# Kernel optimization log

Hardware: AMD Instinct MI355X
Metric: run time of the kernel (lower is better)

Reference implementation:

```python
import jax, jax.numpy as jnp
import numpy as np

T, B = 128, 256      # seq_len, batch
D = 1024             # input_dim (embedding dim)
H = 1024             # hidden_dim
NQ = 8               # n_qubits
V = 32000            # vocab_size
TAGS = 1024          # tagset_size


def setup_inputs() -> dict:
    key = jax.random.key(0)
    ks = jax.random.split(key, 10)
    s = 0.05
    return {
        "sentence": jax.random.randint(ks[0], (T, B), 0, V),
        "emb": jax.random.normal(ks[1], (V, D), jnp.float32) * s,
        # gate order: forget, input, update, output (stacked on leading axis)
        "Wg": jax.random.normal(ks[2], (4, D + H, NQ), jnp.float32) * s,
        "bg": jax.random.normal(ks[3], (4, NQ), jnp.float32) * s,
        "theta": jax.random.normal(ks[4], (4, NQ), jnp.float32) * s,  # trainable RX angles
        "Wp": jax.random.normal(ks[5], (4, NQ, H), jnp.float32) * s,
        "bp": jax.random.normal(ks[6], (4, H), jnp.float32) * s,
        "W_tag": jax.random.normal(ks[7], (H, TAGS), jnp.float32) * s,
        "b_tag": jax.random.normal(ks[8], (TAGS,), jnp.float32) * s,
    }


def reference(sentence, emb, Wg, bg, theta, Wp, bp, W_tag, b_tag):
    embeds = emb[sentence]                      # (T, B, D)
    bsz = embeds.shape[1]
    hidden = Wp.shape[2]

    def step(carry, x):
        hx, cx = carry
        comb = jnp.concatenate([x, hx], axis=1)                       # (B, D+H)
        raw = jnp.einsum('bc,gcq->gbq', comb, Wg) + bg[:, None, :]    # (4, B, NQ)
        # QLayer: RX(x) then trainable RX(theta) per wire on |0>, measure Z
        # -> product state, <Z_i> = cos(raw_i + theta_i)  (exact)
        q = jnp.cos(raw + theta[:, None, :])                          # (4, B, NQ)
        proj = jnp.einsum('gbq,gqh->gbh', q, Wp) + bp[:, None, :]     # (4, B, H)
        f = jax.nn.sigmoid(proj[0])
        i = jax.nn.sigmoid(proj[1])
        g = jnp.tanh(proj[2])
        o = jax.nn.sigmoid(proj[3])
        cx = f * cx + i * g
        hx = o * jnp.tanh(cx)
        return (hx, cx), hx

    hx0 = jnp.zeros((bsz, hidden), embeds.dtype)
    cx0 = jnp.zeros((bsz, hidden), embeds.dtype)
    _, lstm_out = jax.lax.scan(step, (hx0, cx0), embeds)              # (T, B, H)
    tag_logits = lstm_out @ W_tag + b_tag                             # (T, B, TAGS)
    # torch applies log_softmax over dim=1 (the batch axis) -- faithful
    return jax.nn.log_softmax(tag_logits, axis=1)
```

## Files before the change

kernel.cpp:

```cpp
#include <hip/hip_runtime.h>
#include <hip/hip_bf16.h>
#include <stdint.h>

#define T_LEN 128
#define B_SZ  256
#define D_IN  1024
#define H_DIM 1024
#define NQ    8
#define VOCAB 32000
#define TAGS  1024

typedef __attribute__((ext_vector_type(8))) short short8;
typedef __attribute__((ext_vector_type(4))) float f32x4;

__device__ __forceinline__ unsigned short f2bf_bits(float x) {
    __hip_bfloat16 h = __float2bfloat16(x);
    unsigned short u; __builtin_memcpy(&u, &h, 2); return u;
}
__device__ __forceinline__ uint32_t pack_bf2(float a, float b) {
    return (uint32_t)f2bf_bits(a) | ((uint32_t)f2bf_bits(b) << 16);
}
__device__ __forceinline__ float sigmoid_f(float x) {
    return 1.f / (1.f + __expf(-x));
}
__device__ __forceinline__ float tanh_f(float x) {
    return 1.f - 2.f / (__expf(2.f * x) + 1.f);
}
__device__ __forceinline__ void gload_lds16(void* lds_base, const void* gptr) {
    __builtin_amdgcn_global_load_lds(
        (__attribute__((address_space(1))) const void*)gptr,
        (__attribute__((address_space(3))) void*)lds_base,
        16, 0, 0);
}

__global__ __launch_bounds__(256) void k_wt_transpose(const float* __restrict__ W,
                                                      __hip_bfloat16* __restrict__ WtT) {
    __shared__ float tile[32][33];
    const int kb = blockIdx.x * 32, nb = blockIdx.y * 32;
    const int r = threadIdx.x >> 5, c = threadIdx.x & 31;
#pragma unroll
    for (int i = 0; i < 4; ++i)
        tile[r + 8 * i][c] = W[(size_t)(kb + r + 8 * i) * TAGS + nb + c];
    __syncthreads();
#pragma unroll
    for (int i = 0; i < 4; ++i)
        WtT[(size_t)(nb + r + 8 * i) * H_DIM + kb + c] = __float2bfloat16(tile[c][r + 8 * i]);
}

#define GXB_ROWS 32
__global__ __launch_bounds__(256, 2) void k_gx(
    const int* __restrict__ sent, const float* __restrict__ emb,
    const float* __restrict__ Wg, const float* __restrict__ bg,
    const float* __restrict__ theta, float* __restrict__ gx)
{
    __shared__ float xs[2][1024];
    const int tid = threadIdx.x, lane = tid & 63, wv = tid >> 6;
    const int ol = lane & 7, s = lane >> 3;
    const int o = wv * 8 + ol;

    float wk[128];
#pragma unroll
    for (int k = 0; k < 32; ++k)
#pragma unroll
        for (int e = 0; e < 4; ++e) {
            const int c = (s + 8 * k) * 4 + e;
            wk[4 * k + e] = Wg[((size_t)wv * 2048 + c) * 8 + ol];
        }
    const float bt = bg[o] + theta[o];

    const int rbase = blockIdx.x * GXB_ROWS;
    const float4* emb4 = (const float4*)emb;
    float4 xn = emb4[(size_t)sent[rbase] * 256 + tid];
    *(float4*)&xs[0][4 * tid] = xn;
    __syncthreads();

    int cur = 0;
    for (int i8 = 0; i8 < GXB_ROWS / 8; ++i8) {
        float gacc[8];
#pragma unroll
        for (int ii = 0; ii < 8; ++ii) {
            const int i = i8 * 8 + ii;
            const bool havenext = (i + 1 < GXB_ROWS);
            if (havenext)
                xn = emb4[(size_t)sent[rbase + i + 1] * 256 + tid];

            const float4* x4 = (const float4*)xs[cur];
            float a0 = 0.f, a1 = 0.f, a2 = 0.f, a3 = 0.f;
#pragma unroll
            for (int k = 0; k < 32; ++k) {
                float4 v = x4[s + 8 * k];
                a0 = fmaf(wk[4 * k + 0], v.x, a0);
                a1 = fmaf(wk[4 * k + 1], v.y, a1);
                a2 = fmaf(wk[4 * k + 2], v.z, a2);
                a3 = fmaf(wk[4 * k + 3], v.w, a3);
            }
            float a = (a0 + a1) + (a2 + a3);
#pragma unroll
            for (int d = 8; d < 64; d <<= 1) a += __shfl_xor(a, d, 64);
            gacc[ii] = a + bt;

            if (havenext)
                *(float4*)&xs[cur ^ 1][4 * tid] = xn;
            __syncthreads();
            cur ^= 1;
        }
        if (lane < 8) {
#pragma unroll
            for (int ii = 0; ii < 8; ++ii)
                gx[(size_t)(rbase + i8 * 8 + ii) * 32 + wv * 8 + lane] = gacc[ii];
        }
    }
}

__global__ __launch_bounds__(256, 1) void k_qlstm(
    const float* __restrict__ gx, const float* __restrict__ Wg,
    const float* __restrict__ Wp, const float* __restrict__ bp,
    __hip_bfloat16* __restrict__ hb)
{
    __shared__ uint32_t hsb[512];
    __shared__ float red[4 * 36];
    __shared__ float gxl[T_LEN * 32];

    const int tid = threadIdx.x, lane = tid & 63, wv = tid >> 6;
    const int b = blockIdx.x;
    const int lg = lane >> 4;
    const int K0 = wv * 256;
    const int ol = lane & 31;

    union { short8 s8; uint32_t u[4]; } wf[2][8];
#pragma unroll
    for (int ro = 0; ro < 2; ++ro) {
        const int o = ro * 16 + (lane & 15);
        const int g = o >> 3, q = o & 7;
#pragma unroll
        for (int kt = 0; kt < 8; ++kt) {
            const int k0 = K0 + kt * 32 + lg * 8;
#pragma unroll
            for (int p = 0; p < 4; ++p) {
                float e0 = Wg[((size_t)g * 2048 + 1024 + k0 + 2 * p) * 8 + q];
                float e1 = Wg[((size_t)g * 2048 + 1024 + k0 + 2 * p + 1) * 8 + q];
                wf[ro][kt].u[p] = pack_bf2(e0, e1);
            }
        }
    }
    float wpv[4][32], bpv[4][4];
#pragma unroll
    for (int hh = 0; hh < 4; ++hh) {
#pragma unroll
        for (int j = 0; j < 32; ++j)
            wpv[hh][j] = Wp[(size_t)j * H_DIM + 4 * tid + hh];
#pragma unroll
        for (int gg = 0; gg < 4; ++gg)
            bpv[hh][gg] = bp[gg * H_DIM + 4 * tid + hh];
    }

    for (int i = tid; i < T_LEN * 32; i += 256)
        gxl[i] = gx[((size_t)(i >> 5) * B_SZ + b) * 32 + (i & 31)];

    *(uint2*)&hsb[2 * tid] = (uint2){0u, 0u};
    float cx0 = 0.f, cx1 = 0.f, cx2 = 0.f, cx3 = 0.f;
    __syncthreads();

    const f32x4 zf = (f32x4){0.f, 0.f, 0.f, 0.f};

    for (int t8 = 0; t8 < T_LEN / 8; ++t8) {
        uint2 hv8[8];
#pragma unroll
        for (int tt = 0; tt < 8; ++tt) {
            const int t = t8 * 8 + tt;

            f32x4 p0a = zf, p0b = zf, p1a = zf, p1b = zf;
#pragma unroll
            for (int kt = 0; kt < 8; kt += 2) {
                short8 bfA = *(const short8*)((const char*)hsb + 2 * K0 + 64 * kt + lg * 16);
                short8 bfB = *(const short8*)((const char*)hsb + 2 * K0 + 64 * (kt + 1) + lg * 16);
                p0a = __builtin_amdgcn_mfma_f32_16x16x32_bf16(wf[0][kt].s8, bfA, p0a, 0, 0, 0);
                p1a = __builtin_amdgcn_mfma_f32_16x16x32_bf16(wf[1][kt].s8, bfA, p1a, 0, 0, 0);
                p0b = __builtin_amdgcn_mfma_f32_16x16x32_bf16(wf[0][kt + 1].s8, bfB, p0b, 0, 0, 0);
                p1b = __builtin_amdgcn_mfma_f32_16x16x32_bf16(wf[1][kt + 1].s8, bfB, p1b, 0, 0, 0);
            }
            f32x4 p0 = p0a + p0b, p1 = p1a + p1b;
            if ((lane & 15) == 0) {
                *(f32x4*)&red[wv * 36 + 4 * lg] = p0;
                *(f32x4*)&red[wv * 36 + 16 + 4 * lg] = p1;
            }
            __syncthreads();

            float r = gxl[t * 32 + ol]
                    + red[0 * 36 + ol] + red[1 * 36 + ol]
                    + red[2 * 36 + ol] + red[3 * 36 + ol];
            const float qv = __cosf(r);
            float qa[32];
#pragma unroll
            for (int o = 0; o < 32; ++o) qa[o] = __shfl(qv, o, 64);

            float hv[4];
#pragma unroll
            for (int hh = 0; hh < 4; ++hh) {
                float pj[4];
#pragma unroll
                for (int gg = 0; gg < 4; ++gg) {
                    float s = bpv[hh][gg];
#pragma unroll
                    for (int j = 0; j < 8; ++j)
                        s = fmaf(qa[gg * 8 + j], wpv[hh][gg * 8 + j], s);
                    pj[gg] = s;
                }
                const float f_ = sigmoid_f(pj[0]);
                const float i_ = sigmoid_f(pj[1]);
                const float g_ = tanh_f(pj[2]);
                const float o_ = sigmoid_f(pj[3]);
                float& cx = (hh == 0) ? cx0 : (hh == 1) ? cx1 : (hh == 2) ? cx2 : cx3;
                cx = f_ * cx + i_ * g_;
                hv[hh] = o_ * tanh_f(cx);
            }
            const uint2 hvp = (uint2){pack_bf2(hv[0], hv[1]), pack_bf2(hv[2], hv[3])};
            *(uint2*)&hsb[2 * tid] = hvp;
            hv8[tt] = hvp;
            __syncthreads();
        }
#pragma unroll
        for (int tt = 0; tt < 8; ++tt)
            ((uint2*)hb)[((size_t)(t8 * 8 + tt) * B_SZ + b) * 256 + tid] = hv8[tt];
    }
}

__global__ __launch_bounds__(512) void k_tag_gemm_lsm(const __hip_bfloat16* __restrict__ Hb,
                                                      const __hip_bfloat16* __restrict__ WtT,
                                                      float* __restrict__ out)
{
    __shared__ short As[256 * 32];
    __shared__ short Bs[128 * 32];
    __shared__ float wred[8][64];
    __shared__ float wsum[8][64];

    const int t = blockIdx.x, n0 = blockIdx.y * 128;
    const int m0 = t * 256;
    const int tid = threadIdx.x, lane = tid & 63, wid = tid >> 6;
    const int wm = (wid & 3) * 64, wn = (wid >> 2) * 64;
    const int mrow = lane & 15, quad = lane >> 4;
    const int nh = wid >> 2, mw = wid & 3;

    const short* Hs = (const short*)Hb;
    const short* Ws = (const short*)WtT;

    f32x4 acc[4][4];
#pragma unroll
    for (int mi = 0; mi < 4; ++mi)
#pragma unroll
        for (int ni = 0; ni < 4; ++ni)
            acc[mi][ni] = (f32x4){0.f, 0.f, 0.f, 0.f};

    for (int kt = 0; kt < 32; ++kt) {
        const int k0 = kt * 32;
        __syncthreads();
#pragma unroll
        for (int rd = 0; rd < 2; ++rd) {
            const int c = wid + rd * 8;
            const int row = c * 16 + (lane >> 2);
            const int kc = (lane & 3) * 8;
            gload_lds16(&As[c * 512], &Hs[(size_t)(m0 + row) * H_DIM + k0 + kc]);
        }
        {
            const int c = wid;
            const int row = c * 16 + (lane >> 2);
            const int kc = (lane & 3) * 8;
            gload_lds16(&Bs[c * 512], &Ws[(size_t)(n0 + row) * H_DIM + k0 + kc]);
        }
        __syncthreads();

        short8 afr[4], bfr[4];
#pragma unroll
        for (int mi = 0; mi < 4; ++mi)
            afr[mi] = *(const short8*)&As[(wm + mi * 16 + mrow) * 32 + quad * 8];
#pragma unroll
        for (int ni = 0; ni < 4; ++ni)
            bfr[ni] = *(const short8*)&Bs[(wn + ni * 16 + mrow) * 32 + quad * 8];
#pragma unroll
        for (int mi = 0; mi < 4; ++mi)
#pragma unroll
            for (int ni = 0; ni < 4; ++ni)
                acc[mi][ni] = __builtin_amdgcn_mfma_f32_16x16x32_bf16(
                    afr[mi], bfr[ni], acc[mi][ni], 0, 0, 0);
    }

    float cmax[4];
#pragma unroll
    for (int ni = 0; ni < 4; ++ni) {
        float m = -1e30f;
#pragma unroll
        for (int mi = 0; mi < 4; ++mi)
#pragma unroll
            for (int r = 0; r < 4; ++r) m = fmaxf(m, acc[mi][ni][r]);
        m = fmaxf(m, __shfl_xor(m, 16, 64));
        m = fmaxf(m, __shfl_xor(m, 32, 64));
        cmax[ni] = m;
    }
    if (quad == 0) {
#pragma unroll
        for (int ni = 0; ni < 4; ++ni) wred[nh * 4 + mw][ni * 16 + mrow] = cmax[ni];
    }
    __syncthreads();
#pragma unroll
    for (int ni = 0; ni < 4; ++ni) {
        float m = wred[nh * 4 + 0][ni * 16 + mrow];
        m = fmaxf(m, wred[nh * 4 + 1][ni * 16 + mrow]);
        m = fmaxf(m, wred[nh * 4 + 2][ni * 16 + mrow]);
        m = fmaxf(m, wred[nh * 4 + 3][ni * 16 + mrow]);
        cmax[ni] = m;
    }
    float lse[4];
#pragma unroll
    for (int ni = 0; ni < 4; ++ni) {
        float s = 0.f;
#pragma unroll
        for (int mi = 0; mi < 4; ++mi)
#pragma unroll
            for (int r = 0; r < 4; ++r) s += __expf(acc[mi][ni][r] - cmax[ni]);
        s += __shfl_xor(s, 16, 64);
        s += __shfl_xor(s, 32, 64);
        lse[ni] = s;
    }
    if (quad == 0) {
#pragma unroll
        for (int ni = 0; ni < 4; ++ni) wsum[nh * 4 + mw][ni * 16 + mrow] = lse[ni];
    }
    __syncthreads();
#pragma unroll
    for (int ni = 0; ni < 4; ++ni) {
        const float s = wsum[nh * 4 + 0][ni * 16 + mrow]
                      + wsum[nh * 4 + 1][ni * 16 + mrow]
                      + wsum[nh * 4 + 2][ni * 16 + mrow]
                      + wsum[nh * 4 + 3][ni * 16 + mrow];
        lse[ni] = cmax[ni] + __logf(s);
    }
#pragma unroll
    for (int mi = 0; mi < 4; ++mi)
#pragma unroll
        for (int ni = 0; ni < 4; ++ni)
#pragma unroll
            for (int r = 0; r < 4; ++r) {
                const int grow = m0 + wm + mi * 16 + quad * 4 + r;
                const int gcol = n0 + wn + ni * 16 + mrow;
                out[(size_t)grow * TAGS + gcol] = acc[mi][ni][r] - lse[ni];
            }
}

extern "C" void kernel_launch(void* const* d_in, const int* in_sizes, int n_in,
                              void* d_out, int out_size, void* d_ws, size_t ws_size,
                              hipStream_t stream) {
    (void)in_sizes; (void)n_in; (void)out_size; (void)ws_size;
    const int*   sent  = (const int*)d_in[0];
    const float* emb   = (const float*)d_in[1];
    const float* Wg    = (const float*)d_in[2];
    const float* bg    = (const float*)d_in[3];
    const float* theta = (const float*)d_in[4];
    const float* Wp    = (const float*)d_in[5];
    const float* bp    = (const float*)d_in[6];
    const float* Wt    = (const float*)d_in[7];
    float* out = (float*)d_out;

    __hip_bfloat16* hb  = (__hip_bfloat16*)d_ws;
    __hip_bfloat16* WtT = (__hip_bfloat16*)((char*)d_ws + (size_t)64 * 1024 * 1024);
    float* gx = (float*)d_out;

    k_wt_transpose<<<dim3(32, 32), 256, 0, stream>>>(Wt, WtT);
    k_gx<<<dim3((T_LEN * B_SZ) / GXB_ROWS), 256, 0, stream>>>(sent, emb, Wg, bg, theta, gx);
    k_qlstm<<<dim3(B_SZ), 256, 0, stream>>>(gx, Wg, Wp, bp, hb);
    k_tag_gemm_lsm<<<dim3(T_LEN, TAGS / 128), 512, 0, stream>>>(hb, WtT, out);
}
```

Baseline: 574.3 us.

## Double qlstm block to 512 threads, halving per-thread hidden units and K slice

```diff
diff --git a/kernel.cpp b/kernel.cpp
--- a/kernel.cpp
+++ b/kernel.cpp
@@ -112,28 +112,28 @@
     }
 }
 
-__global__ __launch_bounds__(256, 1) void k_qlstm(
+__global__ __launch_bounds__(512, 1) void k_qlstm(
     const float* __restrict__ gx, const float* __restrict__ Wg,
     const float* __restrict__ Wp, const float* __restrict__ bp,
     __hip_bfloat16* __restrict__ hb)
 {
     __shared__ uint32_t hsb[512];
-    __shared__ float red[4 * 36];
+    __shared__ float red[8 * 36];
     __shared__ float gxl[T_LEN * 32];
 
     const int tid = threadIdx.x, lane = tid & 63, wv = tid >> 6;
     const int b = blockIdx.x;
     const int lg = lane >> 4;
-    const int K0 = wv * 256;
+    const int K0 = wv * 128;
     const int ol = lane & 31;
 
-    union { short8 s8; uint32_t u[4]; } wf[2][8];
+    union { short8 s8; uint32_t u[4]; } wf[2][4];
 #pragma unroll
     for (int ro = 0; ro < 2; ++ro) {
         const int o = ro * 16 + (lane & 15);
         const int g = o >> 3, q = o & 7;
 #pragma unroll
-        for (int kt = 0; kt < 8; ++kt) {
+        for (int kt = 0; kt < 4; ++kt) {
             const int k0 = K0 + kt * 32 + lg * 8;
 #pragma unroll
             for (int p = 0; p < 4; ++p) {
@@ -143,35 +143,38 @@
             }
         }
     }
-    float wpv[4][32], bpv[4][4];
-#pragma unroll
-    for (int hh = 0; hh < 4; ++hh) {
-#pragma unroll
-        for (int j = 0; j < 32; ++j)
-            wpv[hh][j] = Wp[(size_t)j * H_DIM + 4 * tid + hh];
-#pragma unroll
-        for (int gg = 0; gg < 4; ++gg)
-            bpv[hh][gg] = bp[gg * H_DIM + 4 * tid + hh];
-    }
-
-    for (int i = tid; i < T_LEN * 32; i += 256)
+    float wpA[32], wpB[32];
+#pragma unroll
+    for (int j = 0; j < 32; ++j) {
+        wpA[j] = Wp[(size_t)j * H_DIM + 2 * tid];
+        wpB[j] = Wp[(size_t)j * H_DIM + 2 * tid + 1];
+    }
+    float bpA[4], bpB[4];
+#pragma unroll
+    for (int gg = 0; gg < 4; ++gg) {
+        bpA[gg] = bp[gg * H_DIM + 2 * tid];
+        bpB[gg] = bp[gg * H_DIM + 2 * tid + 1];
+    }
+
+    for (int i = tid; i < T_LEN * 32; i += 512)
         gxl[i] = gx[((size_t)(i >> 5) * B_SZ + b) * 32 + (i & 31)];
 
-    *(uint2*)&hsb[2 * tid] = (uint2){0u, 0u};
-    float cx0 = 0.f, cx1 = 0.f, cx2 = 0.f, cx3 = 0.f;
-    __syncthreads();
-
+    hsb[tid] = 0u;
+    float cx0 = 0.f, cx1 = 0.f;
+    __syncthreads();
+
+    uint32_t* hb32 = (uint32_t*)hb;
     const f32x4 zf = (f32x4){0.f, 0.f, 0.f, 0.f};
 
     for (int t8 = 0; t8 < T_LEN / 8; ++t8) {
-        uint2 hv8[8];
+        uint32_t hv8[8];
 #pragma unroll
         for (int tt = 0; tt < 8; ++tt) {
             const int t = t8 * 8 + tt;
 
             f32x4 p0a = zf, p0b = zf, p1a = zf, p1b = zf;
 #pragma unroll
-            for (int kt = 0; kt < 8; kt += 2) {
+            for (int kt = 0; kt < 4; kt += 2) {
                 short8 bfA = *(const short8*)((const char*)hsb + 2 * K0 + 64 * kt + lg * 16);
                 short8 bfB = *(const short8*)((const char*)hsb + 2 * K0 + 64 * (kt + 1) + lg * 16);
                 p0a = __builtin_amdgcn_mfma_f32_16x16x32_bf16(wf[0][kt].s8, bfA, p0a, 0, 0, 0);
@@ -186,42 +189,41 @@
             }
             __syncthreads();
 
-            float r = gxl[t * 32 + ol]
-                    + red[0 * 36 + ol] + red[1 * 36 + ol]
-                    + red[2 * 36 + ol] + red[3 * 36 + ol];
+            float r = gxl[t * 32 + ol];
+#pragma unroll
+            for (int w = 0; w < 8; ++w) r += red[w * 36 + ol];
             const float qv = __cosf(r);
             float qa[32];
 #pragma unroll
             for (int o = 0; o < 32; ++o) qa[o] = __shfl(qv, o, 64);
 
-            float hv[4];
-#pragma unroll
-            for (int hh = 0; hh < 4; ++hh) {
-                float pj[4];
-#pragma unroll
-                for (int gg = 0; gg < 4; ++gg) {
-                    float s = bpv[hh][gg];
-#pragma unroll
-                    for (int j = 0; j < 8; ++j)
-                        s = fmaf(qa[gg * 8 + j], wpv[hh][gg * 8 + j], s);
-                    pj[gg] = s;
+            float pjA[4], pjB[4];
+#pragma unroll
+            for (int gg = 0; gg < 4; ++gg) {
+                float sA = bpA[gg], sB = bpB[gg];
+#pragma unroll
+                for (int j = 0; j < 8; ++j) {
+                    sA = fmaf(qa[gg * 8 + j], wpA[gg * 8 + j], sA);
+                    sB = fmaf(qa[gg * 8 + j], wpB[gg * 8 + j], sB);
                 }
-                const float f_ = sigmoid_f(pj[0]);
-                const float i_ = sigmoid_f(pj[1]);
-                const float g_ = tanh_f(pj[2]);
-                const float o_ = sigmoid_f(pj[3]);
-                float& cx = (hh == 0) ? cx0 : (hh == 1) ? cx1 : (hh == 2) ? cx2 : cx3;
-                cx = f_ * cx + i_ * g_;
-                hv[hh] = o_ * tanh_f(cx);
-            }
-            const uint2 hvp = (uint2){pack_bf2(hv[0], hv[1]), pack_bf2(hv[2], hv[3])};
-            *(uint2*)&hsb[2 * tid] = hvp;
+                pjA[gg] = sA; pjB[gg] = sB;
+            }
+            const float fA = sigmoid_f(pjA[0]), iA = sigmoid_f(pjA[1]);
+            const float gA = tanh_f(pjA[2]),   oA = sigmoid_f(pjA[3]);
+            const float fB = sigmoid_f(pjB[0]), iB = sigmoid_f(pjB[1]);
+            const float gB = tanh_f(pjB[2]),   oB = sigmoid_f(pjB[3]);
+            cx0 = fA * cx0 + iA * gA;
+            cx1 = fB * cx1 + iB * gB;
+            const float hv0 = oA * tanh_f(cx0);
+            const float hv1 = oB * tanh_f(cx1);
+            const uint32_t hvp = pack_bf2(hv0, hv1);
+            hsb[tid] = hvp;
             hv8[tt] = hvp;
             __syncthreads();
         }
 #pragma unroll
         for (int tt = 0; tt < 8; ++tt)
-            ((uint2*)hb)[((size_t)(t8 * 8 + tt) * B_SZ + b) * 256 + tid] = hv8[tt];
+            hb32[((size_t)(t8 * 8 + tt) * B_SZ + b) * 512 + tid] = hv8[tt];
     }
 }
 
@@ -366,6 +368,6 @@
 
     k_wt_transpose<<<dim3(32, 32), 256, 0, stream>>>(Wt, WtT);
     k_gx<<<dim3((T_LEN * B_SZ) / GXB_ROWS), 256, 0, stream>>>(sent, emb, Wg, bg, theta, gx);
-    k_qlstm<<<dim3(B_SZ), 256, 0, stream>>>(gx, Wg, Wp, bp, hb);
+    k_qlstm<<<dim3(B_SZ), 512, 0, stream>>>(gx, Wg, Wp, bp, hb);
     k_tag_gemm_lsm<<<dim3(T_LEN, TAGS / 128), 512, 0, stream>>>(hb, WtT, out);
 }
```

New measurement: 564.7 us. Within noise of the previous version (-1.7%).
